# Kernel tuning notes

Measured on AMD Instinct MI355X. Metric: run time of the kernel, lower is better.

Reference implementation:

```python
import jax, jax.numpy as jnp
import numpy as np

MEM_DIM = 2048
MEM_FEAT = 512
N_TOKENS = 65536
ALPHA = 0.1
SOFTMAX_SCALE = 10.0


def _l2_normalize(x, axis, eps=1e-12):
    # matches tf.math.l2_normalize: x / sqrt(max(sum(x^2), eps))
    sq = jnp.sum(jnp.square(x), axis=axis, keepdims=True)
    return x * jax.lax.rsqrt(jnp.maximum(sq, eps))


def setup_inputs() -> dict:
    key = jax.random.key(0)
    k1, k2 = jax.random.split(key)
    inputs = jax.random.normal(k1, (N_TOKENS, MEM_FEAT), dtype=jnp.float32)
    memory = jax.random.normal(k2, (MEM_DIM, MEM_FEAT), dtype=jnp.float32) * 0.05
    return {"inputs": inputs, "memory": memory}


def reference(inputs, memory):
    inputs_norm = _l2_normalize(inputs, axis=1)            # [N, F]
    memory_norm = _l2_normalize(memory, axis=1)            # [M, F]
    cos_sim = jnp.einsum('nf,mf->nm', inputs_norm, memory_norm)  # [N, M]
    attn = jax.nn.softmax(cos_sim * SOFTMAX_SCALE, axis=1)       # [N, M]
    mem_update = jnp.einsum('nm,mf->nf', attn, memory_norm)      # [N, F]
    closest_idx = jnp.argmax(attn, axis=1)                       # [N]
    # one_hot^T @ inputs_norm == segment-sum of inputs_norm by closest code
    memory_updates = jax.ops.segment_sum(inputs_norm, closest_idx,
                                         num_segments=MEM_DIM)  # [M, F]
    updated_memory = memory * (1.0 - ALPHA) + memory_updates * ALPHA
    return mem_update, updated_memory
```

## Files before the change

### kernel.cpp

```cpp
#include <hip/hip_runtime.h>
#include <stdint.h>

#define N_TOK   65536
#define MDIM    2048
#define FDIM    512
#define SCALE_F 10.0f
#define TAU_BF  1.2e-3f
#define TAU_SP  2e-5f
#define QCAP    8192

typedef __attribute__((ext_vector_type(8))) unsigned short u16x8;
typedef __attribute__((ext_vector_type(4))) unsigned short u16x4;
typedef __attribute__((ext_vector_type(8))) __bf16 bf16x8;
typedef __attribute__((ext_vector_type(4))) float f32x4;

__device__ __forceinline__ unsigned short f2bf(float f) {
  unsigned int u = __builtin_bit_cast(unsigned int, f);
  u += 0x7fffu + ((u >> 16) & 1u);
  return (unsigned short)(u >> 16);
}
__device__ __forceinline__ float bf2f(unsigned short b) {
  return __builtin_bit_cast(float, (unsigned int)b << 16);
}
__device__ __forceinline__ f32x4 mfma16(u16x8 a, u16x8 b, f32x4 c) {
  return __builtin_amdgcn_mfma_f32_16x16x32_bf16(
      __builtin_bit_cast(bf16x8, a), __builtin_bit_cast(bf16x8, b), c, 0, 0, 0);
}
__device__ __forceinline__ void gload16(const unsigned short* g, unsigned short* l) {
  __builtin_amdgcn_global_load_lds(
      (const __attribute__((address_space(1))) unsigned int*)g,
      (__attribute__((address_space(3))) unsigned int*)l,
      16, 0, 0);
}
__device__ __forceinline__ unsigned long long packkey(float x, int col) {
  unsigned u = __builtin_bit_cast(unsigned, x);
  u = (u & 0x80000000u) ? ~u : (u | 0x80000000u);
  return ((unsigned long long)u << 32) | (unsigned)(2048 - col);
}
__device__ __forceinline__ float unpackval(unsigned long long k) {
  unsigned u = (unsigned)(k >> 32);
  u = (u & 0x80000000u) ? (u & 0x7fffffffu) : ~u;
  return __builtin_bit_cast(float, u);
}
__device__ __forceinline__ int unpackcol(unsigned long long k) {
  return 2048 - (int)(k & 0xffffffffu);
}
__device__ __forceinline__ void merge2(unsigned long long& k1, unsigned long long& k2,
                                       unsigned long long o1, unsigned long long o2) {
  if (o1 > k1) { k2 = (k1 > o2) ? k1 : o2; k1 = o1; }
  else if (o1 > k2) { k2 = o1; }
}
__device__ __forceinline__ int sslot(int colslot, int lrow) {
  return colslot ^ (lrow & 7);
}

__global__ __launch_bounds__(64) void zero_k(int* __restrict__ qcount) {
  if (threadIdx.x == 0) *qcount = 0;
}

__global__ __launch_bounds__(64) void prep_memory_k(
    const float* __restrict__ mem, unsigned short* __restrict__ Bh,
    unsigned short* __restrict__ Bl) {
  const int m = blockIdx.x;
  const int lane = threadIdx.x;
  const float* row = mem + (size_t)m * FDIM;
  float4 a = *(const float4*)(row + lane * 4);
  float4 b = *(const float4*)(row + 256 + lane * 4);
  float s = a.x * a.x + a.y * a.y + a.z * a.z + a.w * a.w +
            b.x * b.x + b.y * b.y + b.z * b.z + b.w * b.w;
  #pragma unroll
  for (int off = 1; off < 64; off <<= 1) s += __shfl_xor(s, off);
  const float rn = 1.0f / sqrtf(fmaxf(s, 1e-12f));
  float v[8] = {a.x, a.y, a.z, a.w, b.x, b.y, b.z, b.w};
  #pragma unroll
  for (int h = 0; h < 2; ++h) {
    ushort4 hs, lo;
    #pragma unroll
    for (int q = 0; q < 4; ++q) {
      float x = v[h * 4 + q] * rn;
      unsigned short hb = f2bf(x);
      ((unsigned short*)&hs)[q] = hb;
      ((unsigned short*)&lo)[q] = f2bf(x - bf2f(hb));
    }
    const size_t e = (size_t)m * FDIM + h * 256 + lane * 4;
    *(ushort4*)(Bh + e) = hs;
    *(ushort4*)(Bl + e) = lo;
  }
}

__global__ __launch_bounds__(256) void transpose_k(
    const unsigned short* __restrict__ Bh, unsigned short* __restrict__ Bt) {
  __shared__ unsigned short t[32][33];
  const int m0 = blockIdx.x * 32, f0 = blockIdx.y * 32;
  const int tx = threadIdx.x & 31, ty = threadIdx.x >> 5;
  #pragma unroll
  for (int r = ty; r < 32; r += 8)
    t[r][tx] = Bh[(size_t)(m0 + r) * FDIM + f0 + tx];
  __syncthreads();
  #pragma unroll
  for (int r = ty; r < 32; r += 8)
    Bt[(size_t)(f0 + r) * MDIM + m0 + tx] = t[tx][r];
}

__global__ __launch_bounds__(256) void prep_a_k(
    const float* __restrict__ inp, float* __restrict__ inv_n,
    unsigned short* __restrict__ Ah, int baseRow) {
  const int r = blockIdx.x * 4 + (threadIdx.x >> 6);
  const int lane = threadIdx.x & 63;
  const int grow = baseRow + r;
  const float* x = inp + (size_t)grow * FDIM;
  float4 a = *(const float4*)(x + lane * 4);
  float4 b = *(const float4*)(x + 256 + lane * 4);
  float s = a.x * a.x + a.y * a.y + a.z * a.z + a.w * a.w +
            b.x * b.x + b.y * b.y + b.z * b.z + b.w * b.w;
  #pragma unroll
  for (int off = 1; off < 64; off <<= 1) s += __shfl_xor(s, off);
  const float rn = 1.0f / sqrtf(fmaxf(s, 1e-12f));
  if (lane == 0) inv_n[grow] = rn;
  ushort4 h0, h1;
  h0.x = f2bf(a.x * rn); h0.y = f2bf(a.y * rn);
  h0.z = f2bf(a.z * rn); h0.w = f2bf(a.w * rn);
  h1.x = f2bf(b.x * rn); h1.y = f2bf(b.y * rn);
  h1.z = f2bf(b.z * rn); h1.w = f2bf(b.w * rn);
  *(ushort4*)(Ah + (size_t)r * FDIM + lane * 4) = h0;
  *(ushort4*)(Ah + (size_t)r * FDIM + 256 + lane * 4) = h1;
}

template <int MODE, bool SPLIT, bool SWZ>
__global__ __launch_bounds__(256) void gemm_bt_k(
    const unsigned short* __restrict__ Ah, const unsigned short* __restrict__ Al,
    const unsigned short* __restrict__ Bh, const unsigned short* __restrict__ Bl,
    void* __restrict__ Cv, int N, int K, int nbxLog2,
    const int* __restrict__ qlimit, float* __restrict__ ssum,
    unsigned long long* __restrict__ sk1, unsigned long long* __restrict__ sk2) {
  int wg = blockIdx.x;
  if (SWZ) {
    const int q = gridDim.x >> 3;
    wg = (wg & 7) * q + (wg >> 3);
  }
  const int bx = wg & ((1 << nbxLog2) - 1);
  const int by = wg >> nbxLog2;
  const int m0 = by * 128, n0 = bx * 128;
  if (qlimit) {
    int lim = *qlimit; if (lim > QCAP) lim = QCAP;
    lim = (lim + 127) & ~127;
    if (m0 >= lim) return;
  }
  constexpr int BUF_B = (SPLIT ? 4 : 2) * 8192;
  __shared__ alignas(16) char smem[2 * BUF_B];

  const int tid = threadIdx.x;
  const int lane = tid & 63, wave = tid >> 6;
  const int wr = wave >> 1, wc = wave & 1;
  const int lr = lane & 15, ls = lane >> 4;

  f32x4 acc[4][4] = {};

  const int row0 = wave * 32 + (lane >> 2);
  const int row1 = row0 + 16;
  const int ce = (lane & 3) * 8;
  const unsigned short* gA0 = Ah + (size_t)(m0 + row0) * K + ce;
  const unsigned short* gA1 = Ah + (size_t)(m0 + row1) * K + ce;
  const unsigned short* gB0 = Bh + (size_t)(n0 + row0) * K + ce;
  const unsigned short* gB1 = Bh + (size_t)(n0 + row1) * K + ce;
  const unsigned short* gAl0 = nullptr; const unsigned short* gAl1 = nullptr;
  const unsigned short* gBl0 = nullptr; const unsigned short* gBl1 = nullptr;
  if constexpr (SPLIT) {
    gAl0 = Al + (size_t)(m0 + row0) * K + ce;
    gAl1 = Al + (size_t)(m0 + row1) * K + ce;
    gBl0 = Bl + (size_t)(n0 + row0) * K + ce;
    gBl1 = Bl + (size_t)(n0 + row1) * K + ce;
  }

  auto stage = [&](int buf) {
    char* sb = smem + buf * BUF_B;
    unsigned short* bAh = (unsigned short*)sb;
    unsigned short* bBh = (unsigned short*)(sb + 8192);
    gload16(gA0, &bAh[wave * 1024]); gload16(gA1, &bAh[wave * 1024 + 512]);
    gload16(gB0, &bBh[wave * 1024]); gload16(gB1, &bBh[wave * 1024 + 512]);
    if constexpr (SPLIT) {
      unsigned short* bAl = (unsigned short*)(sb + 16384);
      unsigned short* bBl = (unsigned short*)(sb + 24576);
      gload16(gAl0, &bAl[wave * 1024]); gload16(gAl1, &bAl[wave * 1024 + 512]);
      gload16(gBl0, &bBl[wave * 1024]); gload16(gBl1, &bBl[wave * 1024 + 512]);
    }
    gA0 += 32; gA1 += 32; gB0 += 32; gB1 += 32;
    if constexpr (SPLIT) { gAl0 += 32; gAl1 += 32; gBl0 += 32; gBl1 += 32; }
  };

  const int nk = K >> 5;
  stage(0);
  __syncthreads();
  for (int ks = 0; ks < nk; ++ks) {
    const int cur = ks & 1;
    if (ks + 1 < nk) stage(cur ^ 1);
    const char* sb = smem + cur * BUF_B;
    const unsigned short* cAh = (const unsigned short*)sb;
    const unsigned short* cBh = (const unsigned short*)(sb + 8192);
    u16x8 fa[4], fb[4], fal[4], fbl[4];
    #pragma unroll
    for (int i = 0; i < 4; ++i) {
      const int ra = (wr * 64 + i * 16 + lr) * 32 + ls * 8;
      const int rb = (wc * 64 + i * 16 + lr) * 32 + ls * 8;
      fa[i] = *(const u16x8*)&cAh[ra];
      fb[i] = *(const u16x8*)&cBh[rb];
      if constexpr (SPLIT) {
        fal[i] = *(const u16x8*)&((const unsigned short*)(sb + 16384))[ra];
        fbl[i] = *(const u16x8*)&((const unsigned short*)(sb + 24576))[rb];
      }
    }
    #pragma unroll
    for (int i = 0; i < 4; ++i)
      #pragma unroll
      for (int j = 0; j < 4; ++j) {
        acc[i][j] = mfma16(fa[i], fb[j], acc[i][j]);
        if constexpr (SPLIT) {
          acc[i][j] = mfma16(fal[i], fb[j], acc[i][j]);
          acc[i][j] = mfma16(fa[i], fbl[j], acc[i][j]);
        }
      }
    __syncthreads();
  }

  if constexpr (MODE == 1) {
    unsigned short* P = (unsigned short*)Cv;
    float* sS = (float*)smem;
    #pragma unroll
    for (int ph = 0; ph < 4; ++ph) {
      __syncthreads();
      if (wr == (ph >> 1)) {
        const int ibase = (ph & 1) * 2;
        #pragma unroll
        for (int di = 0; di < 2; ++di)
          #pragma unroll
          for (int q = 0; q < 4; ++q) {
            const int lrow = di * 16 + ls * 4 + q;
            float* sr = &sS[lrow * 128];
            #pragma unroll
            for (int j = 0; j < 4; ++j) {
              const int col = wc * 64 + j * 16 + lr;
              sr[sslot(col >> 2, lrow) * 4 + (col & 3)] = acc[ibase + di][j][q];
            }
          }
      }
      __syncthreads();
      const int lrow = tid >> 3;
      const int h = tid & 7;
      const int grow = m0 + ph * 32 + lrow;
      const float* sr = &sS[lrow * 128];
      float esum = 0.f, m1v = -3.4e38f, m2v = -3.4e38f;
      int c1 = 2047;
      #pragma unroll
      for (int k = 0; k < 4; ++k) {
        const int lslot = k * 8 + h;
        const f32x4 v4 = *(const f32x4*)&sr[sslot(lslot, lrow) * 4];
        unsigned short pk4[4];
        #pragma unroll
        for (int e = 0; e < 4; ++e) {
          const float s = v4[e];
          const int col = n0 + lslot * 4 + e;
          if (s > m1v) { m2v = m1v; m1v = s; c1 = col; }
          else if (s > m2v) { m2v = s; }
          const float ex = __expf(SCALE_F * s);
          esum += ex;
          pk4[e] = f2bf(ex);
        }
        *(u16x4*)&P[(size_t)grow * N + n0 + lslot * 4] = *(u16x4*)pk4;
      }
      unsigned long long k1 = packkey(m1v, c1);
      unsigned long long k2 = packkey(m2v, 2047);
      #pragma unroll
      for (int off = 1; off < 8; off <<= 1) {
        const unsigned long long o1 = __shfl_xor(k1, off);
        const unsigned long long o2 = __shfl_xor(k2, off);
        esum += __shfl_xor(esum, off);
        merge2(k1, k2, o1, o2);
      }
      if (h == 0) {
        const size_t sp = (size_t)grow * 16 + bx;
        ssum[sp] = esum; sk1[sp] = k1; sk2[sp] = k2;
      }
    }
  } else {
    float* C = (float*)Cv;
    #pragma unroll
    for (int i = 0; i < 4; ++i) {
      const int rrow = m0 + wr * 64 + i * 16 + ls * 4;
      #pragma unroll
      for (int j = 0; j < 4; ++j) {
        const int col = n0 + wc * 64 + j * 16 + lr;
        #pragma unroll
        for (int q = 0; q < 4; ++q)
          C[(size_t)(rrow + q) * N + col] = acc[i][j][q];
      }
    }
  }
}

__global__ __launch_bounds__(512) void gemm8p2_k(
    const unsigned short* __restrict__ Am, const unsigned short* __restrict__ Bm,
    float* __restrict__ C, int N, int K,
    const float* __restrict__ rowinv) {
  constexpr int NTT = 32;
  constexpr int NITER = NTT / 2;
  __shared__ alignas(16) char smem[131072];
  int wg = blockIdx.x;
  { const int q = gridDim.x >> 3; wg = (wg & 7) * q + (wg >> 3); }
  const int bx0 = wg & 1;
  const int by = wg >> 1;
  const int m0 = by * 256;
  const int tid = threadIdx.x;
  const int lane = tid & 63, wid = tid >> 6;
  const int wm = wid >> 2, wn = wid & 3;
  const int lr = lane & 15, ls = lane >> 4;
  const int c16 = (lane & 7) ^ (lane >> 3);
  const int lrow8 = lane >> 3;

  f32x4 acc[8][4] = {};
  u16x8 bF[4][2];

  auto stageB = [&](int T, int half) {
    const int ko = T * 64;
    char* dst0 = smem + (T & 1) * 65536 + 32768 + half * 16384;
    #pragma unroll
    for (int c = 0; c < 2; ++c) {
      const int R = (wid * 2 + c) * 8;
      const int rg = bx0 * 256 + half * 128 + R + lrow8;
      gload16(Bm + (size_t)rg * K + ko + c16 * 8,
              (unsigned short*)(dst0 + R * 128));
    }
  };
  auto stageA = [&](int T, int q) {
    const int ko = T * 64;
    const int half = wid >> 2;
    const int R = q * 32 + (wid & 3) * 8;
    char* dst = smem + (T & 1) * 65536 + half * 16384 + R * 128;
    const int rg = m0 + half * 128 + R + lrow8;
    gload16(Am + (size_t)rg * K + ko + c16 * 8, (unsigned short*)dst);
  };
  auto ldsA = [&](int b, int rl, int ks) -> u16x8 {
    const int p = (ks * 4 + ls) ^ (rl & 7);
    return *(const u16x8*)(smem + b * 65536 + wm * 16384 + rl * 128 + p * 16);
  };
  auto ldsB = [&](int b, int rlb, int ks) -> u16x8 {
    const int half = rlb >> 7, rl = rlb & 127;
    const int p = (ks * 4 + ls) ^ (rl & 7);
    return *(const u16x8*)(smem + b * 65536 + 32768 + half * 16384 + rl * 128 + p * 16);
  };

  stageB(0, 0); stageB(0, 1);
  stageA(0, 0); stageA(0, 1); stageA(0, 2); stageA(0, 3);
  stageB(1, 0); stageB(1, 1);
  stageA(1, 0); stageA(1, 1); stageA(1, 2);

  for (int it = 0; it < NITER; ++it) {
    const int T0 = 2 * it, T1 = T0 + 1;
    #pragma unroll
    for (int ph = 0; ph < 8; ++ph) {
      const int tb = (ph < 4) ? 0 : 1;
      const int ql = ph & 3;
      if (ql == 0) {
        if (ph == 4 && it == NITER - 1)
          asm volatile("s_waitcnt vmcnt(0)" ::: "memory");
        else
          asm volatile("s_waitcnt vmcnt(7)" ::: "memory");
        __builtin_amdgcn_sched_barrier(0);
        __builtin_amdgcn_s_barrier();
        #pragma unroll
        for (int nj = 0; nj < 4; ++nj)
          #pragma unroll
          for (int ks = 0; ks < 2; ++ks)
            bF[nj][ks] = ldsB(tb, wn * 64 + nj * 16 + lr, ks);
      } else {
        __builtin_amdgcn_s_barrier();
      }
      u16x8 aF[2][2];
      #pragma unroll
      for (int di = 0; di < 2; ++di)
        #pragma unroll
        for (int ks = 0; ks < 2; ++ks)
          aF[di][ks] = ldsA(tb, ql * 32 + di * 16 + lr, ks);
      if (ph == 0) { if (T1 < NTT) stageA(T1, 3); }
      if (ph == 1) { if (T0 + 2 < NTT) stageB(T0 + 2, 0); }
      if (ph == 2) { if (T0 + 2 < NTT) { stageB(T0 + 2, 1); stageA(T0 + 2, 0); } }
      if (ph == 3) { if (T0 + 2 < NTT) { stageA(T0 + 2, 1); stageA(T0 + 2, 2); } }
      if (ph == 4) { if (T0 + 2 < NTT) stageA(T0 + 2, 3); }
      if (ph == 5) { if (T1 + 2 < NTT) stageB(T1 + 2, 0); }
      if (ph == 6) { if (T1 + 2 < NTT) { stageB(T1 + 2, 1); stageA(T1 + 2, 0); } }
      if (ph == 7) { if (T1 + 2 < NTT) { stageA(T1 + 2, 1); stageA(T1 + 2, 2); } }
      __builtin_amdgcn_s_setprio(1);
      #pragma unroll
      for (int di = 0; di < 2; ++di)
        #pragma unroll
        for (int nj = 0; nj < 4; ++nj)
          #pragma unroll
          for (int ks = 0; ks < 2; ++ks)
            acc[ql * 2 + di][nj] = mfma16(aF[di][ks], bF[nj][ks], acc[ql * 2 + di][nj]);
      __builtin_amdgcn_s_setprio(0);
      __builtin_amdgcn_s_barrier();
    }
  }

  const int n0 = bx0 * 256;
  #pragma unroll
  for (int mi = 0; mi < 8; ++mi) {
    const int rbase = m0 + wm * 128 + mi * 16 + ls * 4;
    #pragma unroll
    for (int q = 0; q < 4; ++q) {
      const float ri = rowinv[rbase + q];
      #pragma unroll
      for (int nj = 0; nj < 4; ++nj) {
        const int col = n0 + wn * 64 + nj * 16 + lr;
        C[(size_t)(rbase + q) * N + col] = acc[mi][nj][q] * ri;
      }
    }
  }
}

__global__ __launch_bounds__(256) void rowstat_k(
    const float* __restrict__ ssum, const unsigned long long* __restrict__ sk1,
    const unsigned long long* __restrict__ sk2, int* __restrict__ idx,
    float* __restrict__ rowinv, int* __restrict__ queue,
    int* __restrict__ qcount, int baseRow) {
  const int row = blockIdx.x * 16 + (threadIdx.x >> 4);
  const int p = threadIdx.x & 15;
  const size_t sp = (size_t)row * 16 + p;
  float sum = ssum[sp];
  unsigned long long k1 = sk1[sp], k2 = sk2[sp];
  #pragma unroll
  for (int off = 1; off < 16; off <<= 1) {
    const unsigned long long o1 = __shfl_xor(k1, off);
    const unsigned long long o2 = __shfl_xor(k2, off);
    sum += __shfl_xor(sum, off);
    merge2(k1, k2, o1, o2);
  }
  if (p == 0) {
    const int tok = baseRow + row;
    idx[tok] = unpackcol(k1);
    rowinv[row] = 1.0f / sum;
    if (unpackval(k1) - unpackval(k2) < TAU_BF) {
      int slot = atomicAdd(qcount, 1);
      if (slot < QCAP) queue[slot] = tok;
    }
  }
}

__global__ __launch_bounds__(256) void gather_prep_k(
    const int* __restrict__ queue, const int* __restrict__ qcount,
    const float* __restrict__ inp, const float* __restrict__ inv_n,
    unsigned short* __restrict__ Qh, unsigned short* __restrict__ Ql) {
  const int w = blockIdx.x * 4 + (threadIdx.x >> 6);
  const int lane = threadIdx.x & 63;
  int cnt = *qcount; if (cnt > QCAP) cnt = QCAP;
  if (w >= cnt) return;
  const int tok = queue[w];
  const float rn = inv_n[tok];
  const float* x = inp + (size_t)tok * FDIM;
  #pragma unroll
  for (int h = 0; h < 2; ++h) {
    float4 xv = *(const float4*)(x + h * 256 + lane * 4);
    float vv[4] = {xv.x, xv.y, xv.z, xv.w};
    ushort4 hs, lo;
    #pragma unroll
    for (int q = 0; q < 4; ++q) {
      float v = vv[q] * rn;
      unsigned short hb = f2bf(v);
      ((unsigned short*)&hs)[q] = hb;
      ((unsigned short*)&lo)[q] = f2bf(v - bf2f(hb));
    }
    const size_t e = (size_t)w * FDIM + h * 256 + lane * 4;
    *(ushort4*)(Qh + e) = hs;
    *(ushort4*)(Ql + e) = lo;
  }
}

__global__ __launch_bounds__(256) void refine2_k(
    const int* __restrict__ queue, const int* __restrict__ qcount,
    const float* __restrict__ Sref, const float* __restrict__ inp,
    const float* __restrict__ mem, int* __restrict__ idx) {
  const int w = blockIdx.x * 4 + (threadIdx.x >> 6);
  const int lane = threadIdx.x & 63;
  int cnt = *qcount; if (cnt > QCAP) cnt = QCAP;
  if (w >= cnt) return;
  const int tok = queue[w];
  const float* srow = Sref + (size_t)w * MDIM;
  float m1 = -3.4e38f, m2 = -3.4e38f;
  int i1 = 0x7fffffff, i2 = 0x7fffffff;
  #pragma unroll
  for (int i = 0; i < 8; ++i) {
    const float4 vv = *(const float4*)(srow + i * 256 + lane * 4);
    const float xs[4] = {vv.x, vv.y, vv.z, vv.w};
    #pragma unroll
    for (int q = 0; q < 4; ++q) {
      const float x = xs[q];
      const int ii = i * 256 + lane * 4 + q;
      if (x > m1 || (x == m1 && ii < i1)) { m2 = m1; i2 = i1; m1 = x; i1 = ii; }
      else if (x > m2 || (x == m2 && ii < i2)) { m2 = x; i2 = ii; }
    }
  }
  #pragma unroll
  for (int off = 1; off < 64; off <<= 1) {
    const float n1 = __shfl_xor(m1, off), n2 = __shfl_xor(m2, off);
    const int j1 = __shfl_xor(i1, off), j2 = __shfl_xor(i2, off);
    if (n1 > m1 || (n1 == m1 && j1 < i1)) {
      if (m1 > n2 || (m1 == n2 && i1 < j2)) { m2 = m1; i2 = i1; }
      else { m2 = n2; i2 = j2; }
      m1 = n1; i1 = j1;
    } else if (n1 > m2 || (n1 == m2 && j1 < i2)) { m2 = n1; i2 = j1; }
  }
  int pick = i1;
  if (m1 - m2 < TAU_SP) {
    const int a = (i1 < i2) ? i1 : i2, b = (i1 < i2) ? i2 : i1;
    const float* x = inp + (size_t)tok * FDIM;
    const float* ma = mem + (size_t)a * FDIM;
    const float* mb = mem + (size_t)b * FDIM;
    double da = 0, db = 0, na = 0, nb = 0;
    #pragma unroll
    for (int j = 0; j < 8; ++j) {
      const int e = lane * 8 + j;
      const double xv = x[e], av = ma[e], bv = mb[e];
      da += xv * av; na += av * av;
      db += xv * bv; nb += bv * bv;
    }
    #pragma unroll
    for (int off = 1; off < 64; off <<= 1) {
      da += __shfl_xor(da, off); na += __shfl_xor(na, off);
      db += __shfl_xor(db, off); nb += __shfl_xor(nb, off);
    }
    const double d1 = da / sqrt(fmax(na, 1e-12));
    const double d2 = db / sqrt(fmax(nb, 1e-12));
    if (d2 > d1) pick = b;
    else pick = a;
  }
  if (lane == 0) idx[tok] = pick;
}

__global__ __launch_bounds__(256) void segsum_k(
    const int* __restrict__ idx, const float* __restrict__ inp,
    const float* __restrict__ inv_n, float* __restrict__ updates) {
  __shared__ int lst[256];
  __shared__ int lcnt;
  const int m = blockIdx.x;
  const int t = threadIdx.x;
  float a0 = 0.f, a1 = 0.f;
  for (int base = 0; base < N_TOK; base += 4096) {
    if (t == 0) lcnt = 0;
    __syncthreads();
    #pragma unroll
    for (int u = 0; u < 4; ++u) {
      const int off4 = (u * 256 + t) * 4;
      const int4 v = *(const int4*)&idx[base + off4];
      if (v.x == m) { int p = atomicAdd(&lcnt, 1); if (p < 256) lst[p] = base + off4 + 0; }
      if (v.y == m) { int p = atomicAdd(&lcnt, 1); if (p < 256) lst[p] = base + off4 + 1; }
      if (v.z == m) { int p = atomicAdd(&lcnt, 1); if (p < 256) lst[p] = base + off4 + 2; }
      if (v.w == m) { int p = atomicAdd(&lcnt, 1); if (p < 256) lst[p] = base + off4 + 3; }
    }
    __syncthreads();
    int c = lcnt; if (c > 256) c = 256;
    if (t == 0 && c > 1) {
      for (int i = 1; i < c; ++i) {
        int key = lst[i], j = i - 1;
        while (j >= 0 && lst[j] > key) { lst[j + 1] = lst[j]; --j; }
        lst[j + 1] = key;
      }
    }
    __syncthreads();
    for (int i = 0; i < c; ++i) {
      const int tok = lst[i];
      const float rn = inv_n[tok];
      const float2 xv = *(const float2*)&inp[(size_t)tok * FDIM + t * 2];
      a0 += xv.x * rn; a1 += xv.y * rn;
    }
    __syncthreads();
  }
  *(float2*)&updates[(size_t)m * FDIM + t * 2] = make_float2(a0, a1);
}

__global__ __launch_bounds__(256) void final_update_k(
    const float* __restrict__ mem, const float* __restrict__ upd,
    float* __restrict__ out) {
  const size_t i = ((size_t)blockIdx.x * 256 + threadIdx.x) * 4;
  float4 m = *(const float4*)(mem + i);
  float4 u = *(const float4*)(upd + i);
  float4 r;
  r.x = m.x * 0.9f + u.x * 0.1f;
  r.y = m.y * 0.9f + u.y * 0.1f;
  r.z = m.z * 0.9f + u.z * 0.1f;
  r.w = m.w * 0.9f + u.w * 0.1f;
  *(float4*)(out + i) = r;
}

extern "C" void kernel_launch(void* const* d_in, const int* in_sizes, int n_in,
                              void* d_out, int out_size, void* d_ws, size_t ws_size,
                              hipStream_t stream) {
  const float* inputs = (const float*)d_in[0];
  const float* memory = (const float*)d_in[1];
  if (n_in >= 2 && in_sizes[0] != N_TOK * FDIM) {
    inputs = (const float*)d_in[1];
    memory = (const float*)d_in[0];
  }
  float* out_mu = (float*)d_out;
  float* out_um = out_mu + (size_t)N_TOK * FDIM;

  char* base = (char*)d_ws;
  size_t off = 0;
  auto take = [&](size_t bytes) -> char* {
    char* p = base + off;
    off = (off + bytes + 255) & ~(size_t)255;
    return p;
  };
  unsigned short* Bh = (unsigned short*)take((size_t)MDIM * FDIM * 2);
  unsigned short* Bl = (unsigned short*)take((size_t)MDIM * FDIM * 2);
  unsigned short* Bt = (unsigned short*)take((size_t)MDIM * FDIM * 2);
  float* inv_n = (float*)take((size_t)N_TOK * 4);
  float* updates = (float*)take((size_t)MDIM * FDIM * 4);
  int* idx = (int*)take((size_t)N_TOK * 4);
  int* queue = (int*)take((size_t)QCAP * 4);
  int* qcount = (int*)take(256);
  unsigned short* Qh = (unsigned short*)take((size_t)QCAP * FDIM * 2);
  unsigned short* Ql = (unsigned short*)take((size_t)QCAP * FDIM * 2);
  float* Sref = (float*)take((size_t)QCAP * MDIM * 4);
  const size_t fixed = off;

  int chunkT = 65536;
  while (chunkT > 2048 && fixed + (size_t)chunkT * 5700 + 8192 > ws_size)
    chunkT >>= 1;
  if (fixed + (size_t)chunkT * 5700 + 8192 > ws_size) return;

  unsigned short* Ah = (unsigned short*)take((size_t)chunkT * FDIM * 2);
  unsigned short* Pbuf = (unsigned short*)take((size_t)chunkT * MDIM * 2);
  float* ssum = (float*)take((size_t)chunkT * 16 * 4);
  unsigned long long* sk1 = (unsigned long long*)take((size_t)chunkT * 16 * 8);
  unsigned long long* sk2 = (unsigned long long*)take((size_t)chunkT * 16 * 8);
  float* rowinv = (float*)take((size_t)chunkT * 4);

  zero_k<<<1, 64, 0, stream>>>(qcount);
  prep_memory_k<<<MDIM, 64, 0, stream>>>(memory, Bh, Bl);
  transpose_k<<<dim3(MDIM / 32, FDIM / 32), 256, 0, stream>>>(Bh, Bt);

  const int nby = chunkT / 128;
  for (int baseRow = 0; baseRow < N_TOK; baseRow += chunkT) {
    prep_a_k<<<chunkT / 4, 256, 0, stream>>>(inputs, inv_n, Ah, baseRow);
    gemm_bt_k<1, false, true><<<16 * nby, 256, 0, stream>>>(
        Ah, nullptr, Bh, nullptr, (void*)Pbuf, MDIM, FDIM, 4, nullptr,
        ssum, sk1, sk2);
    rowstat_k<<<chunkT / 16, 256, 0, stream>>>(
        ssum, sk1, sk2, idx, rowinv, queue, qcount, baseRow);
    gemm8p2_k<<<(chunkT / 256) * 2, 512, 0, stream>>>(
        Pbuf, Bt, out_mu + (size_t)baseRow * FDIM, FDIM, MDIM, rowinv);
  }
  gather_prep_k<<<QCAP / 4, 256, 0, stream>>>(queue, qcount, inputs, inv_n, Qh, Ql);
  gemm_bt_k<0, true, false><<<16 * (QCAP / 128), 256, 0, stream>>>(
      Qh, Ql, Bh, Bl, (void*)Sref, MDIM, FDIM, 4, qcount,
      nullptr, nullptr, nullptr);
  refine2_k<<<QCAP / 4, 256, 0, stream>>>(queue, qcount, Sref, inputs, memory, idx);
  segsum_k<<<MDIM, 256, 0, stream>>>(idx, inputs, inv_n, updates);
  final_update_k<<<(MDIM * FDIM / 4) / 256, 256, 0, stream>>>(memory, updates, out_um);
}
```

Before: 726.3 us.

## Switch GEMM operands from bf16 to fp16 and tighten refinement threshold

Replaces bf16 storage and MFMA with fp16 throughout: normalized inputs, memory, the exp-probability matrix, and the hi/lo split. fp16 has more mantissa bits, so the argmax ambiguity threshold TAU_BF is lowered, which should put fewer tokens on the exact-refinement queue and shrink the fallback GEMM and refine work. It also folds the qcount zeroing into prep_memory_k to drop one launch. The risk is fp16 range: exp(10*s) stays within about e^10, so it fits, but the lo residuals may underflow.

Result: faster. 653.1 us, median of 2 (-10.1%).

```diff
diff --git a/kernel.cpp b/kernel.cpp
--- a/kernel.cpp
+++ b/kernel.cpp
@@ -5,26 +5,24 @@
 #define MDIM    2048
 #define FDIM    512
 #define SCALE_F 10.0f
-#define TAU_BF  1.2e-3f
+#define TAU_BF  3e-4f
 #define TAU_SP  2e-5f
 #define QCAP    8192
 
 typedef __attribute__((ext_vector_type(8))) unsigned short u16x8;
 typedef __attribute__((ext_vector_type(4))) unsigned short u16x4;
-typedef __attribute__((ext_vector_type(8))) __bf16 bf16x8;
+typedef __attribute__((ext_vector_type(8))) _Float16 f16x8;
 typedef __attribute__((ext_vector_type(4))) float f32x4;
 
-__device__ __forceinline__ unsigned short f2bf(float f) {
-  unsigned int u = __builtin_bit_cast(unsigned int, f);
-  u += 0x7fffu + ((u >> 16) & 1u);
-  return (unsigned short)(u >> 16);
-}
-__device__ __forceinline__ float bf2f(unsigned short b) {
-  return __builtin_bit_cast(float, (unsigned int)b << 16);
+__device__ __forceinline__ unsigned short f2h(float f) {
+  return __builtin_bit_cast(unsigned short, (_Float16)f);
+}
+__device__ __forceinline__ float h2f(unsigned short u) {
+  return (float)__builtin_bit_cast(_Float16, u);
 }
 __device__ __forceinline__ f32x4 mfma16(u16x8 a, u16x8 b, f32x4 c) {
-  return __builtin_amdgcn_mfma_f32_16x16x32_bf16(
-      __builtin_bit_cast(bf16x8, a), __builtin_bit_cast(bf16x8, b), c, 0, 0, 0);
+  return __builtin_amdgcn_mfma_f32_16x16x32_f16(
+      __builtin_bit_cast(f16x8, a), __builtin_bit_cast(f16x8, b), c, 0, 0, 0);
 }
 __device__ __forceinline__ void gload16(const unsigned short* g, unsigned short* l) {
   __builtin_amdgcn_global_load_lds(
@@ -54,15 +52,12 @@
   return colslot ^ (lrow & 7);
 }
 
-__global__ __launch_bounds__(64) void zero_k(int* __restrict__ qcount) {
-  if (threadIdx.x == 0) *qcount = 0;
-}
-
 __global__ __launch_bounds__(64) void prep_memory_k(
     const float* __restrict__ mem, unsigned short* __restrict__ Bh,
-    unsigned short* __restrict__ Bl) {
+    unsigned short* __restrict__ Bl, int* __restrict__ qcount) {
   const int m = blockIdx.x;
   const int lane = threadIdx.x;
+  if (m == 0 && lane == 0) *qcount = 0;
   const float* row = mem + (size_t)m * FDIM;
   float4 a = *(const float4*)(row + lane * 4);
   float4 b = *(const float4*)(row + 256 + lane * 4);
@@ -78,9 +73,9 @@
     #pragma unroll
     for (int q = 0; q < 4; ++q) {
       float x = v[h * 4 + q] * rn;
-      unsigned short hb = f2bf(x);
+      unsigned short hb = f2h(x);
       ((unsigned short*)&hs)[q] = hb;
-      ((unsigned short*)&lo)[q] = f2bf(x - bf2f(hb));
+      ((unsigned short*)&lo)[q] = f2h(x - h2f(hb));
     }
     const size_t e = (size_t)m * FDIM + h * 256 + lane * 4;
     *(ushort4*)(Bh + e) = hs;
@@ -118,10 +113,10 @@
   const float rn = 1.0f / sqrtf(fmaxf(s, 1e-12f));
   if (lane == 0) inv_n[grow] = rn;
   ushort4 h0, h1;
-  h0.x = f2bf(a.x * rn); h0.y = f2bf(a.y * rn);
-  h0.z = f2bf(a.z * rn); h0.w = f2bf(a.w * rn);
-  h1.x = f2bf(b.x * rn); h1.y = f2bf(b.y * rn);
-  h1.z = f2bf(b.z * rn); h1.w = f2bf(b.w * rn);
+  h0.x = f2h(a.x * rn); h0.y = f2h(a.y * rn);
+  h0.z = f2h(a.z * rn); h0.w = f2h(a.w * rn);
+  h1.x = f2h(b.x * rn); h1.y = f2h(b.y * rn);
+  h1.z = f2h(b.z * rn); h1.w = f2h(b.w * rn);
   *(ushort4*)(Ah + (size_t)r * FDIM + lane * 4) = h0;
   *(ushort4*)(Ah + (size_t)r * FDIM + 256 + lane * 4) = h1;
 }
@@ -263,7 +258,7 @@
           else if (s > m2v) { m2v = s; }
           const float ex = __expf(SCALE_F * s);
           esum += ex;
-          pk4[e] = f2bf(ex);
+          pk4[e] = f2h(ex);
         }
         *(u16x4*)&P[(size_t)grow * N + n0 + lslot * 4] = *(u16x4*)pk4;
       }
@@ -464,9 +459,9 @@
     #pragma unroll
     for (int q = 0; q < 4; ++q) {
       float v = vv[q] * rn;
-      unsigned short hb = f2bf(v);
+      unsigned short hb = f2h(v);
       ((unsigned short*)&hs)[q] = hb;
-      ((unsigned short*)&lo)[q] = f2bf(v - bf2f(hb));
+      ((unsigned short*)&lo)[q] = f2h(v - h2f(hb));
     }
     const size_t e = (size_t)w * FDIM + h * 256 + lane * 4;
     *(ushort4*)(Qh + e) = hs;
@@ -634,8 +629,7 @@
   unsigned long long* sk2 = (unsigned long long*)take((size_t)chunkT * 16 * 8);
   float* rowinv = (float*)take((size_t)chunkT * 4);
 
-  zero_k<<<1, 64, 0, stream>>>(qcount);
-  prep_memory_k<<<MDIM, 64, 0, stream>>>(memory, Bh, Bl);
+  prep_memory_k<<<MDIM, 64, 0, stream>>>(memory, Bh, Bl, qcount);
   transpose_k<<<dim3(MDIM / 32, FDIM / 32), 256, 0, stream>>>(Bh, Bt);
 
   const int nby = chunkT / 128;
```
